# Kernel optimization log

Measured on AMD Instinct MI355X. Metric: run time of the kernel, lower is better.

Reference implementation:

```python
import jax, jax.numpy as jnp
import numpy as np

B, N, C = 128, 2048, 3
VL, PN = 256, 128  # vector_length, prediction_num
NEG_SLOPE = 0.01   # torch LeakyReLU default
BN_EPS = 1e-5


def _lin(key, fin, fout):
    k1, k2 = jax.random.split(key)
    lim = 1.0 / np.sqrt(fin)
    W = jax.random.uniform(k1, (fin, fout), minval=-lim, maxval=lim, dtype=jnp.float32)
    b = jax.random.uniform(k2, (fout,), minval=-lim, maxval=lim, dtype=jnp.float32)
    return W, b


def setup_inputs() -> dict:
    key = jax.random.key(0)
    ks = jax.random.split(key, 14)
    x = jax.random.normal(ks[0], (B, N, C), dtype=jnp.float32)
    lengths = jnp.maximum(jax.random.randint(ks[1], (B,), 0, N), 1).astype(jnp.int32)
    eps = jax.random.normal(ks[2], (B, VL), dtype=jnp.float32)
    W1, b1 = _lin(ks[3], C, 64)
    W2, b2 = _lin(ks[4], 64, 64)
    W3, b3 = _lin(ks[5], 64, 128)
    W4, b4 = _lin(ks[6], 128, 1024)
    Wf, bf = _lin(ks[7], 1024, 1024)
    Wmu, bmu = _lin(ks[8], 1024, VL)
    Wlv, blv = _lin(ks[9], 1024, VL)
    Wd1, bd1 = _lin(ks[10], VL, 1024)
    Wd2, bd2 = _lin(ks[11], 1024, 1024)
    Wd3, bd3 = _lin(ks[12], 1024, PN * C)
    g1 = jnp.ones((1024,), jnp.float32); be1 = jnp.zeros((1024,), jnp.float32)
    g2 = jnp.ones((1024,), jnp.float32); be2 = jnp.zeros((1024,), jnp.float32)
    return dict(x=x, lengths=lengths, eps=eps,
                W1=W1, b1=b1, W2=W2, b2=b2, W3=W3, b3=b3, W4=W4, b4=b4,
                Wf=Wf, bf=bf, Wmu=Wmu, bmu=bmu, Wlv=Wlv, blv=blv,
                Wd1=Wd1, bd1=bd1, g1=g1, be1=be1,
                Wd2=Wd2, bd2=bd2, g2=g2, be2=be2,
                Wd3=Wd3, bd3=bd3)


def _lrelu(h):
    return jnp.where(h > 0, h, NEG_SLOPE * h)


def _bn(h, g, b):
    # BatchNorm1d in training mode: biased batch stats
    m = h.mean(axis=0)
    v = h.var(axis=0)
    return (h - m) * jax.lax.rsqrt(v + BN_EPS) * g + b


def reference(x, lengths, eps,
              W1, b1, W2, b2, W3, b3, W4, b4,
              Wf, bf, Wmu, bmu, Wlv, blv,
              Wd1, bd1, g1, be1, Wd2, bd2, g2, be2, Wd3, bd3):
    # --- pointnet per-point MLP (batched over padded [B,N,C]) ---
    h = _lrelu(x @ W1 + b1)          # [B,N,64]
    h = _lrelu(h @ W2 + b2)          # [B,N,64]
    h = _lrelu(h @ W3 + b3)          # [B,N,128]
    h = _lrelu(h @ W4 + b4)          # [B,N,1024]
    # masked max over points (ragged -> padded+mask)
    mask = jnp.arange(N)[None, :] < lengths[:, None]   # [B,N]
    h = jnp.where(mask[:, :, None], h, -jnp.inf)
    pooled = jnp.max(h, axis=1)      # [B,1024]
    # --- encoder head ---
    e = _lrelu(pooled @ Wf + bf)
    mu = e @ Wmu + bmu               # [B,VL]
    logvar = e @ Wlv + blv           # [B,VL]
    # --- reparameterize ---
    z = mu + eps * jnp.exp(0.5 * logvar)
    # --- decoder: Linear+BN+LeakyReLU x2, final Linear ---
    d = _lrelu(_bn(z @ Wd1 + bd1, g1, be1))
    d = _lrelu(_bn(d @ Wd2 + bd2, g2, be2))
    y = (d @ Wd3 + bd3).reshape(-1, PN, C)   # [B,PN,C]
    return (y, mu, logvar)
```

## Files before the change

### kernel.cpp

```cpp
#include <hip/hip_runtime.h>
#include <hip/hip_bf16.h>
#include <math.h>

#define NEG_SLOPE 0.01f

typedef short short8 __attribute__((ext_vector_type(8)));
typedef float f32x4 __attribute__((ext_vector_type(4)));

__device__ __forceinline__ float lrelu(float v) { return v > 0.0f ? v : NEG_SLOPE * v; }

__device__ __forceinline__ short f2bf(float f) {
    __hip_bfloat16 h = __float2bfloat16(f);
    return __builtin_bit_cast(short, h);
}

__global__ __launch_bounds__(256) void pack_all(
    const float* __restrict__ W4, const float* __restrict__ Wf,
    const float* __restrict__ Wmu, const float* __restrict__ Wlv,
    const float* __restrict__ Wd1, const float* __restrict__ Wd2,
    const float* __restrict__ Wd3, const float* __restrict__ W2,
    const float* __restrict__ W3,
    short* __restrict__ F4, short* __restrict__ Ff, short* __restrict__ Fmuvl,
    short* __restrict__ Fd1, short* __restrict__ Fd2, short* __restrict__ Fd3,
    short* __restrict__ F2, short* __restrict__ F3)
{
    int bid = blockIdx.x;
    const float* src = nullptr; short* dst = nullptr; int K = 0, N = 0; int muvl = 0;
    if      (bid < 64)   { src = W4;  dst = F4;    K = 128;  N = 1024; }
    else if (bid < 576)  { src = Wf;  dst = Ff;    K = 1024; N = 1024; bid -= 64; }
    else if (bid < 832)  { src = nullptr; dst = Fmuvl; K = 1024; N = 512; muvl = 1; bid -= 576; }
    else if (bid < 960)  { src = Wd1; dst = Fd1;   K = 256;  N = 1024; bid -= 832; }
    else if (bid < 1472) { src = Wd2; dst = Fd2;   K = 1024; N = 1024; bid -= 960; }
    else if (bid < 1664) { src = Wd3; dst = Fd3;   K = 1024; N = 384;  bid -= 1472; }
    else if (bid < 1666) { src = W2;  dst = F2;    K = 64;   N = 64;   bid -= 1664; }
    else                 { src = W3;  dst = F3;    K = 64;   N = 128;  bid -= 1666; }

    const int fragid = bid * 4 + (threadIdx.x >> 6);
    const int lane   = threadIdx.x & 63;
    const int K32    = K >> 5;
    const int t   = fragid / (K32 * 4);
    const int rem = fragid - t * K32 * 4;
    const int ks  = rem >> 2;
    const int n   = rem & 3;
    const int col   = t * 64 + n * 16 + (lane & 15);
    const int kbase = ks * 32 + (lane >> 4) * 8;

    short8 v;
#pragma unroll
    for (int e = 0; e < 8; ++e) {
        float f;
        if (muvl) f = (col < 256) ? Wmu[(size_t)(kbase + e) * 256 + col]
                                  : Wlv[(size_t)(kbase + e) * 256 + col - 256];
        else      f = src[(size_t)(kbase + e) * N + col];
        v[e] = f2bf(f);
    }
    *(short8*)&dst[(size_t)fragid * 512 + lane * 8] = v;
}

__global__ __launch_bounds__(128, 2) void h3_kernel(
    const float* __restrict__ x, const int* __restrict__ lengths,
    const float* __restrict__ W1, const float* __restrict__ b1,
    const float* __restrict__ b2, const float* __restrict__ b3,
    const short* __restrict__ F2, const short* __restrict__ F3,
    short* __restrict__ h3p)
{
    const int tid  = threadIdx.x;
    const int b    = blockIdx.x & 127;
    const int c2   = blockIdx.x >> 7;
    const int lane = tid & 63;
    const int w    = tid >> 6;
    const int g    = c2 * 2 + w;
    const int len  = lengths[b];
    if (g * 64 >= len) return;

    __shared__ short S[16384];
    short* Aw = S + w * 8192;
    const int gid = b * 2048 + g * 64 + lane;

    {
        const float x0 = x[gid * 3 + 0];
        const float x1 = x[gid * 3 + 1];
        const float x2 = x[gid * 3 + 2];
#pragma unroll
        for (int q = 0; q < 8; ++q) {
            short8 pv;
#pragma unroll
            for (int e = 0; e < 8; ++e) {
                int c = q * 8 + e;
                float v = b1[c];
                v = fmaf(x0, W1[c], v);
                v = fmaf(x1, W1[64 + c], v);
                v = fmaf(x2, W1[128 + c], v);
                pv[e] = f2bf(lrelu(v));
            }
            *(short8*)&Aw[lane * 64 + ((q ^ (lane & 7)) * 8)] = pv;
        }
    }

    {
        short8 a2[4][2];
#pragma unroll
        for (int m = 0; m < 4; ++m)
#pragma unroll
            for (int ks = 0; ks < 2; ++ks) {
                int rl = m * 16 + (lane & 15);
                int kch = ks * 4 + (lane >> 4);
                a2[m][ks] = *(const short8*)&Aw[rl * 64 + ((kch ^ (rl & 7)) * 8)];
            }
        short8 b2f[2][4];
#pragma unroll
        for (int ks = 0; ks < 2; ++ks)
#pragma unroll
            for (int n = 0; n < 4; ++n)
                b2f[ks][n] = *(const short8*)&F2[(size_t)(ks * 4 + n) * 512 + lane * 8];

        f32x4 acc2[4][4];
#pragma unroll
        for (int m = 0; m < 4; ++m)
#pragma unroll
            for (int n = 0; n < 4; ++n) acc2[m][n] = 0;
#pragma unroll
        for (int ks = 0; ks < 2; ++ks)
#pragma unroll
            for (int n = 0; n < 4; ++n)
#pragma unroll
                for (int m = 0; m < 4; ++m)
                    acc2[m][n] = __builtin_amdgcn_mfma_f32_16x16x32_bf16(
                        a2[m][ks], b2f[ks][n], acc2[m][n], 0, 0, 0);

#pragma unroll
        for (int n = 0; n < 4; ++n) {
            int col = n * 16 + (lane & 15);
            float bv = b2[col];
            int colch = col >> 3;
#pragma unroll
            for (int m = 0; m < 4; ++m)
#pragma unroll
                for (int r = 0; r < 4; ++r) {
                    int rl = m * 16 + (lane >> 4) * 4 + r;
                    Aw[4096 + rl * 64 + ((colch ^ (rl & 7)) * 8) + (col & 7)] =
                        f2bf(lrelu(acc2[m][n][r] + bv));
                }
        }
    }

    {
        short8 a3[4][2];
#pragma unroll
        for (int m = 0; m < 4; ++m)
#pragma unroll
            for (int ks = 0; ks < 2; ++ks) {
                int rl = m * 16 + (lane & 15);
                int kch = ks * 4 + (lane >> 4);
                a3[m][ks] = *(const short8*)&Aw[4096 + rl * 64 + ((kch ^ (rl & 7)) * 8)];
            }
#pragma unroll
        for (int half = 0; half < 2; ++half) {
            short8 b3f[2][4];
#pragma unroll
            for (int ks = 0; ks < 2; ++ks)
#pragma unroll
                for (int n = 0; n < 4; ++n)
                    b3f[ks][n] = *(const short8*)&F3[(size_t)(half * 8 + ks * 4 + n) * 512 + lane * 8];

            f32x4 acc3[4][4];
#pragma unroll
            for (int m = 0; m < 4; ++m)
#pragma unroll
                for (int n = 0; n < 4; ++n) acc3[m][n] = 0;
#pragma unroll
            for (int ks = 0; ks < 2; ++ks)
#pragma unroll
                for (int n = 0; n < 4; ++n)
#pragma unroll
                    for (int m = 0; m < 4; ++m)
                        acc3[m][n] = __builtin_amdgcn_mfma_f32_16x16x32_bf16(
                            a3[m][ks], b3f[ks][n], acc3[m][n], 0, 0, 0);

#pragma unroll
            for (int n = 0; n < 4; ++n) {
                int col = half * 64 + n * 16 + (lane & 15);
                float bv = b3[col];
                int colch = col >> 3;
#pragma unroll
                for (int m = 0; m < 4; ++m)
#pragma unroll
                    for (int r = 0; r < 4; ++r) {
                        int rl = m * 16 + (lane >> 4) * 4 + r;
                        Aw[rl * 128 + ((colch ^ (rl & 7)) * 8) + (col & 7)] =
                            f2bf(lrelu(acc3[m][n][r] + bv));
                    }
            }
        }
    }

    const size_t obase = ((size_t)(b * 32 + g) * 16) * 512 + lane * 8;
#pragma unroll
    for (int ks = 0; ks < 4; ++ks)
#pragma unroll
        for (int m = 0; m < 4; ++m) {
            int rl = m * 16 + (lane & 15);
            int ch = (ks * 4 + (lane >> 4)) ^ (rl & 7);
            short8 af = *(const short8*)&Aw[rl * 128 + ch * 8];
            *(short8*)&h3p[obase + (size_t)(ks * 4 + m) * 512] = af;
        }
}

__global__ __launch_bounds__(256, 3) void l4_pool_kernel(
    const short* __restrict__ h3p, const int* __restrict__ lengths,
    const short* __restrict__ F4, float* __restrict__ part)
{
    const int tid = threadIdx.x, lane = tid & 63, w = tid >> 6;
    const int bid = blockIdx.x;
    const int ch  = (bid >> 3) & 3;
    const int p   = (bid >> 5) * 8 + (bid & 7);
    const int b   = p & 127;
    const int rs  = p >> 7;

    const int len = lengths[b];
    const int live64 = (len + 63) >> 6;
    const int cbeg = rs * 4;
    int cend = cbeg + 4; if (cend > live64) cend = live64;
    if (cbeg >= cend) return;

    __shared__ short L[16384];

    const int t = ch * 4 + w;
    short8 bfr[4][4];
#pragma unroll
    for (int ks = 0; ks < 4; ++ks)
#pragma unroll
        for (int n = 0; n < 4; ++n)
            bfr[ks][n] = *(const short8*)&F4[(size_t)((t * 4 + ks) * 4 + n) * 512 + lane * 8];

    const int partial = (len & 63) ? (live64 - 1) : -1;
    const int rem = len & 63;

    f32x4 rmax[4];
#pragma unroll
    for (int n = 0; n < 4; ++n)
#pragma unroll
        for (int rr = 0; rr < 4; ++rr) rmax[n][rr] = -INFINITY;

    const size_t bb = (size_t)b * 32;
    short8 stg[4];
    {
        const size_t fb = (bb + cbeg) * 16 * 512;
#pragma unroll
        for (int pass = 0; pass < 4; ++pass)
            stg[pass] = *(const short8*)&h3p[fb + (size_t)(pass * 256 + tid) * 8];
#pragma unroll
        for (int pass = 0; pass < 4; ++pass)
            *(short8*)&L[(pass * 256 + tid) * 8] = stg[pass];
    }
    __syncthreads();

    for (int c = cbeg; c < cend; ++c) {
        const int p2 = (c - cbeg) & 1;
        if (c + 1 < cend) {
            const size_t fb = (bb + c + 1) * 16 * 512;
#pragma unroll
            for (int pass = 0; pass < 4; ++pass)
                stg[pass] = *(const short8*)&h3p[fb + (size_t)(pass * 256 + tid) * 8];
        }

        const short* Lb = L + p2 * 8192;
#pragma unroll
        for (int mh = 0; mh < 2; ++mh) {
            f32x4 acc[2][4];
#pragma unroll
            for (int j = 0; j < 2; ++j)
#pragma unroll
                for (int n = 0; n < 4; ++n) acc[j][n] = 0;
#pragma unroll
            for (int ks = 0; ks < 4; ++ks) {
                short8 a0 = *(const short8*)&Lb[(ks * 4 + mh * 2 + 0) * 512 + lane * 8];
                short8 a1 = *(const short8*)&Lb[(ks * 4 + mh * 2 + 1) * 512 + lane * 8];
#pragma unroll
                for (int n = 0; n < 4; ++n) {
                    acc[0][n] = __builtin_amdgcn_mfma_f32_16x16x32_bf16(a0, bfr[ks][n], acc[0][n], 0, 0, 0);
                    acc[1][n] = __builtin_amdgcn_mfma_f32_16x16x32_bf16(a1, bfr[ks][n], acc[1][n], 0, 0, 0);
                }
            }
            if (c == partial) {
#pragma unroll
                for (int j = 0; j < 2; ++j)
#pragma unroll
                    for (int n = 0; n < 4; ++n)
#pragma unroll
                        for (int rr = 0; rr < 4; ++rr) {
                            int row = mh * 32 + j * 16 + (lane >> 4) * 4 + rr;
                            rmax[n][rr] = fmaxf(rmax[n][rr],
                                (row < rem) ? acc[j][n][rr] : -INFINITY);
                        }
            } else {
#pragma unroll
                for (int j = 0; j < 2; ++j)
#pragma unroll
                    for (int n = 0; n < 4; ++n)
#pragma unroll
                        for (int rr = 0; rr < 4; ++rr)
                            rmax[n][rr] = fmaxf(rmax[n][rr], acc[j][n][rr]);
            }
        }

        if (c + 1 < cend) {
            short* Ln = L + (p2 ^ 1) * 8192;
#pragma unroll
            for (int pass = 0; pass < 4; ++pass)
                *(short8*)&Ln[(pass * 256 + tid) * 8] = stg[pass];
        }
        __syncthreads();
    }

#pragma unroll
    for (int n = 0; n < 4; ++n) {
        float v = fmaxf(fmaxf(rmax[n][0], rmax[n][1]), fmaxf(rmax[n][2], rmax[n][3]));
        v = fmaxf(v, __shfl_xor(v, 16));
        v = fmaxf(v, __shfl_xor(v, 32));
        if (lane < 16)
            part[((size_t)b * 8 + rs) * 1024 + ch * 256 + w * 64 + n * 16 + lane] = v;
    }
}

__global__ __launch_bounds__(256) void reduce_pool_kernel(
    const float* __restrict__ part, const int* __restrict__ lengths,
    const float* __restrict__ b4, short* __restrict__ pooled)
{
    const int b = blockIdx.x;
    const int nlive = (lengths[b] + 255) >> 8;
    for (int i = threadIdx.x; i < 1024; i += 256) {
        float m = part[((size_t)b * 8 + 0) * 1024 + i];
        for (int j = 1; j < nlive; ++j)
            m = fmaxf(m, part[((size_t)b * 8 + j) * 1024 + i]);
        pooled[(size_t)b * 1024 + i] = f2bf(lrelu(m + b4[i]));
    }
}

template<int K32, int EPI>
__global__ __launch_bounds__(64) void gemm16(
    const short* __restrict__ A, const short* __restrict__ Wfrag,
    const float* __restrict__ bias, const float* __restrict__ bias2,
    float* __restrict__ outF, float* __restrict__ outF2,
    short* __restrict__ outB, int Nout)
{
    const int lane = threadIdx.x;
    const int cbb = blockIdx.x, rh = blockIdx.y;
    const int K = K32 * 32;
    const int t = cbb >> 2, n = cbb & 3;

    short8 bf[K32];
#pragma unroll
    for (int ks = 0; ks < K32; ++ks)
        bf[ks] = *(const short8*)&Wfrag[(size_t)((t * K32 + ks) * 4 + n) * 512 + lane * 8];

    const int arow0 = rh * 32 + (lane & 15);
    const int koff  = (lane >> 4) * 8;
    f32x4 acc[2];
    acc[0] = 0; acc[1] = 0;
#pragma unroll
    for (int ks = 0; ks < K32; ++ks) {
        short8 a0 = *(const short8*)&A[(size_t)arow0 * K + ks * 32 + koff];
        short8 a1 = *(const short8*)&A[(size_t)(arow0 + 16) * K + ks * 32 + koff];
        acc[0] = __builtin_amdgcn_mfma_f32_16x16x32_bf16(a0, bf[ks], acc[0], 0, 0, 0);
        acc[1] = __builtin_amdgcn_mfma_f32_16x16x32_bf16(a1, bf[ks], acc[1], 0, 0, 0);
    }

    const int c0 = cbb * 16;
    const int cl = lane & 15;
    if (EPI == 2) {
        const float* bs = (c0 < 256) ? bias : bias2;
        float* of = (c0 < 256) ? outF : outF2;
        int col = (c0 & 255) + cl;
        float bv = bs[col];
#pragma unroll
        for (int m = 0; m < 2; ++m)
#pragma unroll
            for (int rr = 0; rr < 4; ++rr) {
                int row = rh * 32 + m * 16 + (lane >> 4) * 4 + rr;
                of[(size_t)row * 256 + col] = acc[m][rr] + bv;
            }
    } else {
        int col = c0 + cl;
        float bv = bias[col];
#pragma unroll
        for (int m = 0; m < 2; ++m)
#pragma unroll
            for (int rr = 0; rr < 4; ++rr) {
                int row = rh * 32 + m * 16 + (lane >> 4) * 4 + rr;
                float v = acc[m][rr] + bv;
                if (EPI == 1) outB[(size_t)row * Nout + col] = f2bf(lrelu(v));
                else          outF[(size_t)row * Nout + col] = v;
            }
    }
}

template<int K32, bool ZIN>
__global__ __launch_bounds__(256) void gemmBN(
    const short* __restrict__ A, const float* __restrict__ muv,
    const float* __restrict__ lvv, const float* __restrict__ eps,
    const short* __restrict__ Wfrag,
    const float* __restrict__ g, const float* __restrict__ be,
    short* __restrict__ outB, int Nout)
{
    __shared__ float bns[4][16];
    __shared__ float bnq[4][16];

    const int tid = threadIdx.x, lane = tid & 63, w = tid >> 6;
    const int cbb = blockIdx.x;
    const int K = K32 * 32;
    const int t = cbb >> 2, n = cbb & 3;

    short8 bf[K32];
#pragma unroll
    for (int ks = 0; ks < K32; ++ks)
        bf[ks] = *(const short8*)&Wfrag[(size_t)((t * K32 + ks) * 4 + n) * 512 + lane * 8];

    const int arow0 = w * 32 + (lane & 15);
    const int koff  = (lane >> 4) * 8;
    f32x4 acc[2];
    acc[0] = 0; acc[1] = 0;
#pragma unroll
    for (int ks = 0; ks < K32; ++ks) {
        short8 a0, a1;
        if (ZIN) {
#pragma unroll
            for (int e = 0; e < 8; ++e) {
                int k = ks * 32 + koff + e;
                size_t i0 = (size_t)arow0 * 256 + k;
                size_t i1 = (size_t)(arow0 + 16) * 256 + k;
                a0[e] = f2bf(fmaf(eps[i0], expf(0.5f * lvv[i0]), muv[i0]));
                a1[e] = f2bf(fmaf(eps[i1], expf(0.5f * lvv[i1]), muv[i1]));
            }
        } else {
            a0 = *(const short8*)&A[(size_t)arow0 * K + ks * 32 + koff];
            a1 = *(const short8*)&A[(size_t)(arow0 + 16) * K + ks * 32 + koff];
        }
        acc[0] = __builtin_amdgcn_mfma_f32_16x16x32_bf16(a0, bf[ks], acc[0], 0, 0, 0);
        acc[1] = __builtin_amdgcn_mfma_f32_16x16x32_bf16(a1, bf[ks], acc[1], 0, 0, 0);
    }

    float s = 0.f, q = 0.f;
#pragma unroll
    for (int m = 0; m < 2; ++m)
#pragma unroll
        for (int rr = 0; rr < 4; ++rr) {
            float v = acc[m][rr];
            s += v; q = fmaf(v, v, q);
        }
    s += __shfl_xor(s, 16); s += __shfl_xor(s, 32);
    q += __shfl_xor(q, 16); q += __shfl_xor(q, 32);
    if (lane < 16) { bns[w][lane] = s; bnq[w][lane] = q; }
    __syncthreads();

    const int cl = lane & 15;
    float st = bns[0][cl] + bns[1][cl] + bns[2][cl] + bns[3][cl];
    float qt = bnq[0][cl] + bnq[1][cl] + bnq[2][cl] + bnq[3][cl];
    float mean = st * (1.0f / 128.0f);
    float var  = qt * (1.0f / 128.0f) - mean * mean;
    float rs   = 1.0f / sqrtf(var + 1e-5f);
    const int col = cbb * 16 + cl;
    float gg = g[col] * rs;
    float bb = be[col] - mean * gg;

#pragma unroll
    for (int m = 0; m < 2; ++m)
#pragma unroll
        for (int rr = 0; rr < 4; ++rr) {
            int row = w * 32 + m * 16 + (lane >> 4) * 4 + rr;
            outB[(size_t)row * Nout + col] = f2bf(lrelu(fmaf(acc[m][rr], gg, bb)));
        }
}

extern "C" void kernel_launch(void* const* d_in, const int* in_sizes, int n_in,
                              void* d_out, int out_size, void* d_ws, size_t ws_size,
                              hipStream_t stream)
{
    const float* x       = (const float*)d_in[0];
    const int*   lengths = (const int*)  d_in[1];
    const float* eps     = (const float*)d_in[2];
    const float* W1  = (const float*)d_in[3];  const float* b1  = (const float*)d_in[4];
    const float* W2  = (const float*)d_in[5];  const float* b2  = (const float*)d_in[6];
    const float* W3  = (const float*)d_in[7];  const float* b3  = (const float*)d_in[8];
    const float* W4  = (const float*)d_in[9];  const float* b4  = (const float*)d_in[10];
    const float* Wf  = (const float*)d_in[11]; const float* bf  = (const float*)d_in[12];
    const float* Wmu = (const float*)d_in[13]; const float* bmu = (const float*)d_in[14];
    const float* Wlv = (const float*)d_in[15]; const float* blv = (const float*)d_in[16];
    const float* Wd1 = (const float*)d_in[17];
    const float* g1  = (const float*)d_in[19]; const float* be1 = (const float*)d_in[20];
    const float* Wd2 = (const float*)d_in[21];
    const float* g2  = (const float*)d_in[23]; const float* be2 = (const float*)d_in[24];
    const float* Wd3 = (const float*)d_in[25]; const float* bd3 = (const float*)d_in[26];

    float* out = (float*)d_out;
    float* y_out  = out;
    float* mu_out = out + 49152;
    float* lv_out = out + 81920;

    char* ws = (char*)d_ws;
    short* F4    = (short*)(ws + 0);
    short* Ff    = (short*)(ws + 262144);
    short* Fmuvl = (short*)(ws + 2359296);
    short* Fd1   = (short*)(ws + 3407872);
    short* Fd2   = (short*)(ws + 3932160);
    short* Fd3   = (short*)(ws + 6029312);
    short* F2    = (short*)(ws + 6815744);
    short* F3    = (short*)(ws + 6823936);
    short* h3p   = (short*)(ws + 6840320);
    float* part  = (float*)(ws + 73949184);
    short* pooled = (short*)(ws + 6840320 + 0);
    short* ebuf   = (short*)(ws + 6840320 + 262144);
    short* d1v    = (short*)(ws + 6840320 + 524288);
    short* d2v    = (short*)(ws + 6840320 + 786432);

    pack_all<<<1670, 256, 0, stream>>>(W4, Wf, Wmu, Wlv, Wd1, Wd2, Wd3, W2, W3,
                                       F4, Ff, Fmuvl, Fd1, Fd2, Fd3, F2, F3);
    h3_kernel<<<2048, 128, 0, stream>>>(x, lengths, W1, b1, b2, b3, F2, F3, h3p);
    l4_pool_kernel<<<4096, 256, 0, stream>>>(h3p, lengths, F4, part);
    reduce_pool_kernel<<<128, 256, 0, stream>>>(part, lengths, b4, pooled);
    gemm16<32, 1><<<dim3(64, 4), 64, 0, stream>>>(pooled, Ff, bf, nullptr,
                                                  nullptr, nullptr, ebuf, 1024);
    gemm16<32, 2><<<dim3(32, 4), 64, 0, stream>>>(ebuf, Fmuvl, bmu, blv,
                                                  mu_out, lv_out, nullptr, 256);
    gemmBN<8, true><<<64, 256, 0, stream>>>(nullptr, mu_out, lv_out, eps,
                                            Fd1, g1, be1, d1v, 1024);
    gemmBN<32, false><<<64, 256, 0, stream>>>(d1v, nullptr, nullptr, nullptr,
                                              Fd2, g2, be2, d2v, 1024);
    gemm16<32, 0><<<dim3(24, 4), 64, 0, stream>>>(d2v, Fd3, bd3, nullptr,
                                                  y_out, nullptr, nullptr, 384);
}
```

Baseline: 121.7 us.

## Fuse pool-reduce and MLP tail GEMMs into one cooperative kernel with grid syncs

Replaces the reduce-pool kernel and five small GEMM launches (encoder fc, mu/logvar, two BN decoder layers, final linear) with a single 128-block cooperative kernel that separates the stages with grid.sync(). The aim is to remove per-launch overhead and inter-kernel gaps for these tiny latency-bound GEMMs. Weight fragments are now loaded per k-step instead of being preloaded into registers, and some stages leave most blocks or waves idle. The l4_pool grid is also remapped to a 3D grid (b, ch, rs), which changes the block scheduling order.

```diff
diff --git a/kernel.cpp b/kernel.cpp
--- a/kernel.cpp
+++ b/kernel.cpp
@@ -1,6 +1,9 @@
 #include <hip/hip_runtime.h>
 #include <hip/hip_bf16.h>
+#include <hip/hip_cooperative_groups.h>
 #include <math.h>
+
+namespace cg = cooperative_groups;
 
 #define NEG_SLOPE 0.01f
 
@@ -211,12 +214,7 @@
     const short* __restrict__ F4, float* __restrict__ part)
 {
     const int tid = threadIdx.x, lane = tid & 63, w = tid >> 6;
-    const int bid = blockIdx.x;
-    const int ch  = (bid >> 3) & 3;
-    const int p   = (bid >> 5) * 8 + (bid & 7);
-    const int b   = p & 127;
-    const int rs  = p >> 7;
-
+    const int b = blockIdx.x, ch = blockIdx.y, rs = blockIdx.z;
     const int len = lengths[b];
     const int live64 = (len + 63) >> 6;
     const int cbeg = rs * 4;
@@ -323,153 +321,199 @@
     }
 }
 
-__global__ __launch_bounds__(256) void reduce_pool_kernel(
+__global__ __launch_bounds__(256) void tail_coop(
     const float* __restrict__ part, const int* __restrict__ lengths,
-    const float* __restrict__ b4, short* __restrict__ pooled)
+    const float* __restrict__ b4,
+    const short* __restrict__ Ff, const float* __restrict__ bfv,
+    const short* __restrict__ Fmuvl, const float* __restrict__ bmu,
+    const float* __restrict__ blv, const float* __restrict__ eps,
+    const short* __restrict__ Fd1, const float* __restrict__ g1,
+    const float* __restrict__ be1,
+    const short* __restrict__ Fd2, const float* __restrict__ g2,
+    const float* __restrict__ be2,
+    const short* __restrict__ Fd3, const float* __restrict__ bd3,
+    short* __restrict__ pooled, short* __restrict__ ebuf,
+    short* __restrict__ d1v, short* __restrict__ d2v,
+    float* __restrict__ mu_out, float* __restrict__ lv_out,
+    float* __restrict__ y_out)
 {
-    const int b = blockIdx.x;
-    const int nlive = (lengths[b] + 255) >> 8;
-    for (int i = threadIdx.x; i < 1024; i += 256) {
-        float m = part[((size_t)b * 8 + 0) * 1024 + i];
-        for (int j = 1; j < nlive; ++j)
-            m = fmaxf(m, part[((size_t)b * 8 + j) * 1024 + i]);
-        pooled[(size_t)b * 1024 + i] = f2bf(lrelu(m + b4[i]));
-    }
-}
-
-template<int K32, int EPI>
-__global__ __launch_bounds__(64) void gemm16(
-    const short* __restrict__ A, const short* __restrict__ Wfrag,
-    const float* __restrict__ bias, const float* __restrict__ bias2,
-    float* __restrict__ outF, float* __restrict__ outF2,
-    short* __restrict__ outB, int Nout)
-{
-    const int lane = threadIdx.x;
-    const int cbb = blockIdx.x, rh = blockIdx.y;
-    const int K = K32 * 32;
-    const int t = cbb >> 2, n = cbb & 3;
-
-    short8 bf[K32];
-#pragma unroll
-    for (int ks = 0; ks < K32; ++ks)
-        bf[ks] = *(const short8*)&Wfrag[(size_t)((t * K32 + ks) * 4 + n) * 512 + lane * 8];
-
-    const int arow0 = rh * 32 + (lane & 15);
-    const int koff  = (lane >> 4) * 8;
-    f32x4 acc[2];
-    acc[0] = 0; acc[1] = 0;
-#pragma unroll
-    for (int ks = 0; ks < K32; ++ks) {
-        short8 a0 = *(const short8*)&A[(size_t)arow0 * K + ks * 32 + koff];
-        short8 a1 = *(const short8*)&A[(size_t)(arow0 + 16) * K + ks * 32 + koff];
-        acc[0] = __builtin_amdgcn_mfma_f32_16x16x32_bf16(a0, bf[ks], acc[0], 0, 0, 0);
-        acc[1] = __builtin_amdgcn_mfma_f32_16x16x32_bf16(a1, bf[ks], acc[1], 0, 0, 0);
-    }
-
-    const int c0 = cbb * 16;
-    const int cl = lane & 15;
-    if (EPI == 2) {
-        const float* bs = (c0 < 256) ? bias : bias2;
-        float* of = (c0 < 256) ? outF : outF2;
-        int col = (c0 & 255) + cl;
-        float bv = bs[col];
-#pragma unroll
-        for (int m = 0; m < 2; ++m)
-#pragma unroll
-            for (int rr = 0; rr < 4; ++rr) {
-                int row = rh * 32 + m * 16 + (lane >> 4) * 4 + rr;
-                of[(size_t)row * 256 + col] = acc[m][rr] + bv;
-            }
-    } else {
-        int col = c0 + cl;
-        float bv = bias[col];
-#pragma unroll
-        for (int m = 0; m < 2; ++m)
-#pragma unroll
-            for (int rr = 0; rr < 4; ++rr) {
-                int row = rh * 32 + m * 16 + (lane >> 4) * 4 + rr;
-                float v = acc[m][rr] + bv;
-                if (EPI == 1) outB[(size_t)row * Nout + col] = f2bf(lrelu(v));
-                else          outF[(size_t)row * Nout + col] = v;
-            }
-    }
-}
-
-template<int K32, bool ZIN>
-__global__ __launch_bounds__(256) void gemmBN(
-    const short* __restrict__ A, const float* __restrict__ muv,
-    const float* __restrict__ lvv, const float* __restrict__ eps,
-    const short* __restrict__ Wfrag,
-    const float* __restrict__ g, const float* __restrict__ be,
-    short* __restrict__ outB, int Nout)
-{
+    cg::grid_group grid = cg::this_grid();
+    const int bid = blockIdx.x;
+    const int tid = threadIdx.x, lane = tid & 63, w = tid >> 6;
+
     __shared__ float bns[4][16];
     __shared__ float bnq[4][16];
 
-    const int tid = threadIdx.x, lane = tid & 63, w = tid >> 6;
-    const int cbb = blockIdx.x;
-    const int K = K32 * 32;
-    const int t = cbb >> 2, n = cbb & 3;
-
-    short8 bf[K32];
-#pragma unroll
-    for (int ks = 0; ks < K32; ++ks)
-        bf[ks] = *(const short8*)&Wfrag[(size_t)((t * K32 + ks) * 4 + n) * 512 + lane * 8];
-
-    const int arow0 = w * 32 + (lane & 15);
-    const int koff  = (lane >> 4) * 8;
-    f32x4 acc[2];
-    acc[0] = 0; acc[1] = 0;
-#pragma unroll
-    for (int ks = 0; ks < K32; ++ks) {
-        short8 a0, a1;
-        if (ZIN) {
+    {
+        const int b = bid;
+        const int nlive = (lengths[b] + 255) >> 8;
+        for (int i = tid; i < 1024; i += 256) {
+            float m = part[((size_t)b * 8 + 0) * 1024 + i];
+            for (int j = 1; j < nlive; ++j)
+                m = fmaxf(m, part[((size_t)b * 8 + j) * 1024 + i]);
+            pooled[(size_t)b * 1024 + i] = f2bf(lrelu(m + b4[i]));
+        }
+    }
+    grid.sync();
+
+    {
+        const int cb = bid & 63, rh = bid >> 6;
+        const int arow = rh * 64 + w * 16 + (lane & 15);
+        const int koff = (lane >> 4) * 8;
+        const int t = cb >> 2, n = cb & 3;
+        f32x4 acc = 0;
+#pragma unroll
+        for (int ks = 0; ks < 32; ++ks) {
+            short8 a  = *(const short8*)&pooled[(size_t)arow * 1024 + ks * 32 + koff];
+            short8 bB = *(const short8*)&Ff[((size_t)(t * 32 + ks) * 4 + n) * 512 + lane * 8];
+            acc = __builtin_amdgcn_mfma_f32_16x16x32_bf16(a, bB, acc, 0, 0, 0);
+        }
+        int col = cb * 16 + (lane & 15);
+        float bv = bfv[col];
+#pragma unroll
+        for (int rr = 0; rr < 4; ++rr) {
+            int row = rh * 64 + w * 16 + (lane >> 4) * 4 + rr;
+            ebuf[(size_t)row * 1024 + col] = f2bf(lrelu(acc[rr] + bv));
+        }
+    }
+    grid.sync();
+
+    if (w == 0) {
+        const int cb = bid & 15, rq = bid >> 4;
+        const int arow = rq * 16 + (lane & 15);
+        const int koff = (lane >> 4) * 8;
+        const int t = cb >> 2, n = cb & 3;
+        f32x4 macc = 0, lacc = 0;
+#pragma unroll
+        for (int ks = 0; ks < 32; ++ks) {
+            short8 a  = *(const short8*)&ebuf[(size_t)arow * 1024 + ks * 32 + koff];
+            short8 bm = *(const short8*)&Fmuvl[((size_t)(t * 32 + ks) * 4 + n) * 512 + lane * 8];
+            short8 bl = *(const short8*)&Fmuvl[((size_t)((t + 4) * 32 + ks) * 4 + n) * 512 + lane * 8];
+            macc = __builtin_amdgcn_mfma_f32_16x16x32_bf16(a, bm, macc, 0, 0, 0);
+            lacc = __builtin_amdgcn_mfma_f32_16x16x32_bf16(a, bl, lacc, 0, 0, 0);
+        }
+        int col = cb * 16 + (lane & 15);
+        float bmv = bmu[col], blvv = blv[col];
+#pragma unroll
+        for (int rr = 0; rr < 4; ++rr) {
+            int row = rq * 16 + (lane >> 4) * 4 + rr;
+            mu_out[(size_t)row * 256 + col] = macc[rr] + bmv;
+            lv_out[(size_t)row * 256 + col] = lacc[rr] + blvv;
+        }
+    }
+    grid.sync();
+
+    if (bid < 64) {
+        const int cbb = bid;
+        const int t = cbb >> 2, n = cbb & 3;
+        const int arow0 = w * 32 + (lane & 15);
+        const int koff  = (lane >> 4) * 8;
+        f32x4 acc[2]; acc[0] = 0; acc[1] = 0;
+#pragma unroll
+        for (int ks = 0; ks < 8; ++ks) {
+            short8 a0, a1;
 #pragma unroll
             for (int e = 0; e < 8; ++e) {
                 int k = ks * 32 + koff + e;
                 size_t i0 = (size_t)arow0 * 256 + k;
                 size_t i1 = (size_t)(arow0 + 16) * 256 + k;
-                a0[e] = f2bf(fmaf(eps[i0], expf(0.5f * lvv[i0]), muv[i0]));
-                a1[e] = f2bf(fmaf(eps[i1], expf(0.5f * lvv[i1]), muv[i1]));
-            }
-        } else {
-            a0 = *(const short8*)&A[(size_t)arow0 * K + ks * 32 + koff];
-            a1 = *(const short8*)&A[(size_t)(arow0 + 16) * K + ks * 32 + koff];
-        }
-        acc[0] = __builtin_amdgcn_mfma_f32_16x16x32_bf16(a0, bf[ks], acc[0], 0, 0, 0);
-        acc[1] = __builtin_amdgcn_mfma_f32_16x16x32_bf16(a1, bf[ks], acc[1], 0, 0, 0);
-    }
-
-    float s = 0.f, q = 0.f;
-#pragma unroll
-    for (int m = 0; m < 2; ++m)
+                a0[e] = f2bf(fmaf(eps[i0], expf(0.5f * lv_out[i0]), mu_out[i0]));
+                a1[e] = f2bf(fmaf(eps[i1], expf(0.5f * lv_out[i1]), mu_out[i1]));
+            }
+            short8 bB = *(const short8*)&Fd1[((size_t)(t * 8 + ks) * 4 + n) * 512 + lane * 8];
+            acc[0] = __builtin_amdgcn_mfma_f32_16x16x32_bf16(a0, bB, acc[0], 0, 0, 0);
+            acc[1] = __builtin_amdgcn_mfma_f32_16x16x32_bf16(a1, bB, acc[1], 0, 0, 0);
+        }
+        float s = 0.f, q = 0.f;
+#pragma unroll
+        for (int m = 0; m < 2; ++m)
+#pragma unroll
+            for (int rr = 0; rr < 4; ++rr) { float v = acc[m][rr]; s += v; q = fmaf(v, v, q); }
+        s += __shfl_xor(s, 16); s += __shfl_xor(s, 32);
+        q += __shfl_xor(q, 16); q += __shfl_xor(q, 32);
+        if (lane < 16) { bns[w][lane] = s; bnq[w][lane] = q; }
+        __syncthreads();
+        const int cl = lane & 15;
+        float st = bns[0][cl] + bns[1][cl] + bns[2][cl] + bns[3][cl];
+        float qt = bnq[0][cl] + bnq[1][cl] + bnq[2][cl] + bnq[3][cl];
+        float mean = st * (1.0f / 128.0f);
+        float var  = qt * (1.0f / 128.0f) - mean * mean;
+        float rs   = 1.0f / sqrtf(var + 1e-5f);
+        const int col = cbb * 16 + cl;
+        float gg = g1[col] * rs;
+        float bb = be1[col] - mean * gg;
+#pragma unroll
+        for (int m = 0; m < 2; ++m)
+#pragma unroll
+            for (int rr = 0; rr < 4; ++rr) {
+                int row = w * 32 + m * 16 + (lane >> 4) * 4 + rr;
+                d1v[(size_t)row * 1024 + col] = f2bf(lrelu(fmaf(acc[m][rr], gg, bb)));
+            }
+    }
+    grid.sync();
+
+    if (bid < 64) {
+        const int cbb = bid;
+        const int t = cbb >> 2, n = cbb & 3;
+        const int arow0 = w * 32 + (lane & 15);
+        const int koff  = (lane >> 4) * 8;
+        f32x4 acc[2]; acc[0] = 0; acc[1] = 0;
+#pragma unroll
+        for (int ks = 0; ks < 32; ++ks) {
+            short8 a0 = *(const short8*)&d1v[(size_t)arow0 * 1024 + ks * 32 + koff];
+            short8 a1 = *(const short8*)&d1v[(size_t)(arow0 + 16) * 1024 + ks * 32 + koff];
+            short8 bB = *(const short8*)&Fd2[((size_t)(t * 32 + ks) * 4 + n) * 512 + lane * 8];
+            acc[0] = __builtin_amdgcn_mfma_f32_16x16x32_bf16(a0, bB, acc[0], 0, 0, 0);
+            acc[1] = __builtin_amdgcn_mfma_f32_16x16x32_bf16(a1, bB, acc[1], 0, 0, 0);
+        }
+        float s = 0.f, q = 0.f;
+#pragma unroll
+        for (int m = 0; m < 2; ++m)
+#pragma unroll
+            for (int rr = 0; rr < 4; ++rr) { float v = acc[m][rr]; s += v; q = fmaf(v, v, q); }
+        s += __shfl_xor(s, 16); s += __shfl_xor(s, 32);
+        q += __shfl_xor(q, 16); q += __shfl_xor(q, 32);
+        if (lane < 16) { bns[w][lane] = s; bnq[w][lane] = q; }
+        __syncthreads();
+        const int cl = lane & 15;
+        float st = bns[0][cl] + bns[1][cl] + bns[2][cl] + bns[3][cl];
+        float qt = bnq[0][cl] + bnq[1][cl] + bnq[2][cl] + bnq[3][cl];
+        float mean = st * (1.0f / 128.0f);
+        float var  = qt * (1.0f / 128.0f) - mean * mean;
+        float rs   = 1.0f / sqrtf(var + 1e-5f);
+        const int col = cbb * 16 + cl;
+        float gg = g2[col] * rs;
+        float bb = be2[col] - mean * gg;
+#pragma unroll
+        for (int m = 0; m < 2; ++m)
+#pragma unroll
+            for (int rr = 0; rr < 4; ++rr) {
+                int row = w * 32 + m * 16 + (lane >> 4) * 4 + rr;
+                d2v[(size_t)row * 1024 + col] = f2bf(lrelu(fmaf(acc[m][rr], gg, bb)));
+            }
+    }
+    grid.sync();
+
+    if (bid < 96 && w < 2) {
+        const int cbb = bid % 24, rh = bid / 24;
+        const int t = cbb >> 2, n = cbb & 3;
+        const int arow = rh * 32 + w * 16 + (lane & 15);
+        const int koff = (lane >> 4) * 8;
+        f32x4 acc = 0;
+#pragma unroll
+        for (int ks = 0; ks < 32; ++ks) {
+            short8 a  = *(const short8*)&d2v[(size_t)arow * 1024 + ks * 32 + koff];
+            short8 bB = *(const short8*)&Fd3[((size_t)(t * 32 + ks) * 4 + n) * 512 + lane * 8];
+            acc = __builtin_amdgcn_mfma_f32_16x16x32_bf16(a, bB, acc, 0, 0, 0);
+        }
+        int col = cbb * 16 + (lane & 15);
+        float bv = bd3[col];
 #pragma unroll
         for (int rr = 0; rr < 4; ++rr) {
-            float v = acc[m][rr];
-            s += v; q = fmaf(v, v, q);
-        }
-    s += __shfl_xor(s, 16); s += __shfl_xor(s, 32);
-    q += __shfl_xor(q, 16); q += __shfl_xor(q, 32);
-    if (lane < 16) { bns[w][lane] = s; bnq[w][lane] = q; }
-    __syncthreads();
-
-    const int cl = lane & 15;
-    float st = bns[0][cl] + bns[1][cl] + bns[2][cl] + bns[3][cl];
-    float qt = bnq[0][cl] + bnq[1][cl] + bnq[2][cl] + bnq[3][cl];
-    float mean = st * (1.0f / 128.0f);
-    float var  = qt * (1.0f / 128.0f) - mean * mean;
-    float rs   = 1.0f / sqrtf(var + 1e-5f);
-    const int col = cbb * 16 + cl;
-    float gg = g[col] * rs;
-    float bb = be[col] - mean * gg;
-
-#pragma unroll
-    for (int m = 0; m < 2; ++m)
-#pragma unroll
-        for (int rr = 0; rr < 4; ++rr) {
-            int row = w * 32 + m * 16 + (lane >> 4) * 4 + rr;
-            outB[(size_t)row * Nout + col] = f2bf(lrelu(fmaf(acc[m][rr], gg, bb)));
-        }
+            int row = rh * 32 + w * 16 + (lane >> 4) * 4 + rr;
+            y_out[(size_t)row * 384 + col] = acc[rr] + bv;
+        }
+    }
 }
 
 extern "C" void kernel_launch(void* const* d_in, const int* in_sizes, int n_in,
@@ -516,16 +560,17 @@
     pack_all<<<1670, 256, 0, stream>>>(W4, Wf, Wmu, Wlv, Wd1, Wd2, Wd3, W2, W3,
                                        F4, Ff, Fmuvl, Fd1, Fd2, Fd3, F2, F3);
     h3_kernel<<<2048, 128, 0, stream>>>(x, lengths, W1, b1, b2, b3, F2, F3, h3p);
-    l4_pool_kernel<<<4096, 256, 0, stream>>>(h3p, lengths, F4, part);
-    reduce_pool_kernel<<<128, 256, 0, stream>>>(part, lengths, b4, pooled);
-    gemm16<32, 1><<<dim3(64, 4), 64, 0, stream>>>(pooled, Ff, bf, nullptr,
-                                                  nullptr, nullptr, ebuf, 1024);
-    gemm16<32, 2><<<dim3(32, 4), 64, 0, stream>>>(ebuf, Fmuvl, bmu, blv,
-                                                  mu_out, lv_out, nullptr, 256);
-    gemmBN<8, true><<<64, 256, 0, stream>>>(nullptr, mu_out, lv_out, eps,
-                                            Fd1, g1, be1, d1v, 1024);
-    gemmBN<32, false><<<64, 256, 0, stream>>>(d1v, nullptr, nullptr, nullptr,
-                                              Fd2, g2, be2, d2v, 1024);
-    gemm16<32, 0><<<dim3(24, 4), 64, 0, stream>>>(d2v, Fd3, bd3, nullptr,
-                                                  y_out, nullptr, nullptr, 384);
+    l4_pool_kernel<<<dim3(128, 4, 8), 256, 0, stream>>>(h3p, lengths, F4, part);
+    void* args[] = {
+        (void*)&part, (void*)&lengths, (void*)&b4,
+        (void*)&Ff, (void*)&bf,
+        (void*)&Fmuvl, (void*)&bmu, (void*)&blv, (void*)&eps,
+        (void*)&Fd1, (void*)&g1, (void*)&be1,
+        (void*)&Fd2, (void*)&g2, (void*)&be2,
+        (void*)&Fd3, (void*)&bd3,
+        (void*)&pooled, (void*)&ebuf, (void*)&d1v, (void*)&d2v,
+        (void*)&mu_out, (void*)&lv_out, (void*)&y_out
+    };
+    hipLaunchCooperativeKernel((void*)tail_coop, dim3(128), dim3(256),
+                               args, 0, stream);
 }
```

Measured after the change: 207.6 us. 70.6% more time.
